# Performance work log

Measured on AMD Instinct MI355X. Metric: run time of the kernel, lower is better.

Reference implementation:

```python
import jax, jax.numpy as jnp
import numpy as np

SR = 44100
WT_LEN = 512
N_WT = 20
B, T = 16, 262144


def setup_inputs() -> dict:
    key = jax.random.key(0)
    k1, k2, k3, k4 = jax.random.split(key, 4)
    # realistic fundamental frequencies in [50, 500) Hz
    pitch = 50.0 + 450.0 * jax.random.uniform(k1, (B, T, 1), dtype=jnp.float32)
    amplitude = jax.random.uniform(k2, (B, T, 1), dtype=jnp.float32)
    attention = jax.random.uniform(k3, (B, T, N_WT), dtype=jnp.float32)
    # learned wavetables [N_WT, WT_LEN]; first 4 are fixed sine cycles, rest learnable noise
    i = np.arange(WT_LEN, dtype=np.float32)
    sines = np.stack([np.sin((c + 1) * 2 * np.pi * i / WT_LEN) for c in range(4)]).astype(np.float32)
    rest = 0.01 * np.asarray(jax.random.normal(k4, (N_WT - 4, WT_LEN)), dtype=np.float32)
    wt = np.concatenate([sines, rest], axis=0)
    # module enforces wt[-1] == wt[0] (periodic closure)
    wt[:, -1] = wt[:, 0]
    return {"pitch": pitch, "amplitude": amplitude, "attention": attention,
            "wavetables": jnp.asarray(wt)}


def reference(pitch, amplitude, attention, wavetables):
    L = wavetables.shape[1]
    # tanh applied to learnable tables only (indices >= 4)
    wt = jnp.concatenate([wavetables[:4], jnp.tanh(wavetables[4:])], axis=0)  # [K, L]
    freq = pitch[..., 0]                                   # [B, T]
    increment = freq / SR * L                              # [B, T]
    index = jnp.cumsum(increment, axis=-1) - increment[:, :1]
    index = index % L
    idx_low = jnp.floor(index)
    idx_high = jnp.ceil(index)
    alpha = index - idx_low                                # [B, T]
    il = idx_low.astype(jnp.int32)
    ih = (idx_high.astype(jnp.int32)) % L
    wt_t = wt.T                                            # [L, K]
    low = wt_t[il]                                         # [B, T, K] single gather for all tables
    high = wt_t[ih]                                        # [B, T, K]
    waveforms = low + alpha[..., None] * (high - low)      # [B, T, K]
    mixed = jnp.sum(waveforms * attention, axis=-1)        # [B, T]
    return (mixed[..., None] * amplitude)                  # [B, T, 1]
```

## Files before the change

kernel.cpp:

```cpp
#include <hip/hip_runtime.h>
#include <math.h>

#define WT_LEN 512
#define N_WT 20
#define B_ 16
#define T_ 262144
#define TOTAL (B_ * T_)
#define CHUNK 8192
#define NCHR 32
#define NCH  512
#define DTHREADS 1024

__device__ __forceinline__ float to_inc1(float x) {
    return (x / 44100.0f) * 512.0f;
}
__device__ __forceinline__ float4 to_inc4(float4 p) {
    float4 r;
    r.x = to_inc1(p.x); r.y = to_inc1(p.y);
    r.z = to_inc1(p.z); r.w = to_inc1(p.w);
    return r;
}

template <bool STORE_INC>
__global__ __launch_bounds__(DTHREADS) void up_kernel(
        const float* __restrict__ pitch, float* __restrict__ A13,
        float* __restrict__ incbuf) {
    __shared__ float red[2048];
    const int t = threadIdx.x;
    const size_t g0 = (size_t)blockIdx.x * CHUNK;

    const float4* p4 = (const float4*)(pitch + g0);
    float4 v0 = to_inc4(p4[2 * t]);
    float4 v1 = to_inc4(p4[2 * t + 1]);
    if (STORE_INC) {
        float4* q4 = (float4*)(incbuf + g0);
        q4[2 * t] = v0; q4[2 * t + 1] = v1;
    }
    float t0 = v0.x + v0.y, t1 = v0.z + v0.w;
    float t2 = v1.x + v1.y, t3 = v1.z + v1.w;
    red[t] = (t0 + t1) + (t2 + t3);
    __syncthreads();
    int off_prev = 0, off = 1024;
    for (int sz = 512; sz >= 1; sz >>= 1) {
        if (t < sz) red[off + t] = red[off_prev + 2 * t] + red[off_prev + 2 * t + 1];
        __syncthreads();
        off_prev = off; off += sz;
    }
    if (t == 0) A13[blockIdx.x] = red[2046];
}

__global__ void mid_kernel(const float* __restrict__ A13,
                           const float* __restrict__ pitch,
                           float* __restrict__ S13, float* __restrict__ X0) {
    int r = threadIdx.x;
    if (r >= B_) return;
    float l0[32], l1[16], l2[8], l3[4], l4[2], l5;
    for (int i = 0; i < 32; ++i) l0[i] = A13[r * 32 + i];
    for (int i = 0; i < 16; ++i) l1[i] = l0[2 * i] + l0[2 * i + 1];
    for (int i = 0; i < 8;  ++i) l2[i] = l1[2 * i] + l1[2 * i + 1];
    for (int i = 0; i < 4;  ++i) l3[i] = l2[2 * i] + l2[2 * i + 1];
    for (int i = 0; i < 2;  ++i) l4[i] = l3[2 * i] + l3[2 * i + 1];
    l5 = l4[0] + l4[1];

    float s4[2], s3[4], s2[8], s1[16], s0[32];
    s4[0] = l4[0]; s4[1] = l5;
    s3[0] = l3[0];
    for (int i = 0; i < 2; ++i) {
        s3[2 * i + 1] = s4[i];
        if (2 * i + 2 < 4) s3[2 * i + 2] = s4[i] + l3[2 * i + 2];
    }
    s2[0] = l2[0];
    for (int i = 0; i < 4; ++i) {
        s2[2 * i + 1] = s3[i];
        if (2 * i + 2 < 8) s2[2 * i + 2] = s3[i] + l2[2 * i + 2];
    }
    s1[0] = l1[0];
    for (int i = 0; i < 8; ++i) {
        s1[2 * i + 1] = s2[i];
        if (2 * i + 2 < 16) s1[2 * i + 2] = s2[i] + l1[2 * i + 2];
    }
    s0[0] = l0[0];
    for (int i = 0; i < 16; ++i) {
        s0[2 * i + 1] = s1[i];
        if (2 * i + 2 < 32) s0[2 * i + 2] = s1[i] + l0[2 * i + 2];
    }
    for (int i = 0; i < 32; ++i) S13[r * 32 + i] = s0[i];
    X0[r] = to_inc1(pitch[(size_t)r * T_]);
}

__constant__ int OFF[14] = {0, 8192, 12288, 14336, 15360, 15872, 16128,
                            16256, 16320, 16352, 16368, 16376, 16380, 16382};

template <bool FROM_INC>
__global__ __launch_bounds__(DTHREADS) void down_kernel(
        const float* __restrict__ src,
        const float* __restrict__ S13,
        float* __restrict__ sout) {
    __shared__ float a[16384];
    const int t = threadIdx.x;
    const size_t g0 = (size_t)blockIdx.x * CHUNK;

    const float4* p4 = (const float4*)(src + g0);
    float4 v0 = p4[2 * t], v1 = p4[2 * t + 1];
    if (!FROM_INC) { v0 = to_inc4(v0); v1 = to_inc4(v1); }
    ((float4*)a)[2 * t] = v0;
    ((float4*)a)[2 * t + 1] = v1;
    __syncthreads();

    for (int k = 1; k <= 12; ++k) {
        int m = CHUNK >> k;
        int bp = OFF[k - 1], b = OFF[k];
        for (int i = t; i < m; i += DTHREADS)
            a[b + i] = a[bp + 2 * i] + a[bp + 2 * i + 1];
        __syncthreads();
    }

    const float P = (blockIdx.x & (NCHR - 1)) ? S13[blockIdx.x - 1] : 0.0f;
    const float T13 = S13[blockIdx.x];

    if (t == 0) {
        a[OFF[12]]     = P + a[OFF[12]];
        a[OFF[12] + 1] = T13;
    }
    __syncthreads();
    for (int k = 11; k >= 0; --k) {
        int m = CHUNK >> k, half = m >> 1;
        int b = OFF[k], bn = OFF[k + 1];
        for (int i = t; i < half; i += DTHREADS) {
            float sn = a[bn + i];
            int j = 2 * i + 2;
            float av = (j < m) ? a[b + j] : 0.0f;
            a[b + 2 * i + 1] = sn;
            if (j < m) a[b + j] = sn + av;
        }
        if (t == 0) a[b] = P + a[b];
        __syncthreads();
    }

    float4* q4 = (float4*)(sout + g0);
    q4[2 * t]     = ((float4*)a)[2 * t];
    q4[2 * t + 1] = ((float4*)a)[2 * t + 1];
}

__global__ __launch_bounds__(256) void mix_kernel(
        float* io, const float* __restrict__ X0,
        const float* __restrict__ amp, const float* __restrict__ att,
        const float* __restrict__ wtg, int total) {
    __shared__ float wt_lds[WT_LEN * N_WT];
    for (int e = threadIdx.x; e < WT_LEN * N_WT; e += blockDim.x) {
        int c = e / WT_LEN;
        int i = e - c * WT_LEN;
        float v = wtg[e];
        if (c >= 4) v = tanhf(v);
        wt_lds[i * N_WT + c] = v;
    }
    __syncthreads();

    int gid = blockIdx.x * blockDim.x + threadIdx.x;
    if (gid >= total) return;

    int row = gid >> 18;
    float S  = io[gid];
    float y  = S - X0[row];

    float qf  = floorf(y * (1.0f / 512.0f));
    float idx = fmaf(-512.0f, qf, y);
    if (idx < 0.0f)    idx += 512.0f;
    if (idx >= 512.0f) idx -= 512.0f;

    float fl0   = floorf(idx);
    float alpha = idx - fl0;
    int il = ((int)fl0) & (WT_LEN - 1);
    int ih = (il + (alpha > 0.0f ? 1 : 0)) & (WT_LEN - 1);

    const float4* lo4 = (const float4*)(&wt_lds[il * N_WT]);
    const float4* hi4 = (const float4*)(&wt_lds[ih * N_WT]);
    const float4* a4  = (const float4*)(att + (size_t)gid * N_WT);

    float acc = 0.0f;
#pragma unroll
    for (int v = 0; v < 5; ++v) {
        float4 lo = lo4[v];
        float4 hi = hi4[v];
        float4 at = a4[v];
        acc += at.x * (lo.x + alpha * (hi.x - lo.x));
        acc += at.y * (lo.y + alpha * (hi.y - lo.y));
        acc += at.z * (lo.z + alpha * (hi.z - lo.z));
        acc += at.w * (lo.w + alpha * (hi.w - lo.w));
    }
    io[gid] = acc * amp[gid];
}

extern "C" void kernel_launch(void* const* d_in, const int* in_sizes, int n_in,
                              void* d_out, int out_size, void* d_ws, size_t ws_size,
                              hipStream_t stream) {
    const float* pitch = (const float*)d_in[0];
    const float* amp   = (const float*)d_in[1];
    const float* att   = (const float*)d_in[2];
    const float* wtg   = (const float*)d_in[3];
    float* S = (float*)d_out;

    float* A13 = (float*)d_ws;
    float* S13 = A13 + NCH;
    float* X0  = S13 + NCH;
    float* INC = A13 + 4096;
    const bool use_inc =
        ws_size >= (size_t)(4096 + TOTAL) * sizeof(float);

    if (use_inc) {
        up_kernel<true><<<NCH, DTHREADS, 0, stream>>>(pitch, A13, INC);
        mid_kernel<<<1, 64, 0, stream>>>(A13, pitch, S13, X0);
        down_kernel<true><<<NCH, DTHREADS, 0, stream>>>(INC, S13, S);
    } else {
        up_kernel<false><<<NCH, DTHREADS, 0, stream>>>(pitch, A13, nullptr);
        mid_kernel<<<1, 64, 0, stream>>>(A13, pitch, S13, X0);
        down_kernel<false><<<NCH, DTHREADS, 0, stream>>>(pitch, S13, S);
    }
    mix_kernel<<<(TOTAL + 255) / 256, 256, 0, stream>>>(S, X0, amp, att, wtg,
                                                        TOTAL);
}
```

Baseline: 565.0 us.

## Restructure scan to per-thread register sums and precompute wavetable once

The down-sweep scan now keeps each thread's 8 increments in registers and scans only the 1024 per-thread partial sums in a 2048-float LDS buffer, instead of a full 16K-float LDS tree over 8192 elements. The INC intermediate buffer is dropped, so pitch is reread and converted on the fly rather than written and reread. Wavetable tanh and transpose move into the single-block mid kernel, which writes them to workspace. The mix kernel becomes a persistent grid of 1024 blocks of 512 threads that bulk-copies the prepared table into LDS once per block. These changes aim to cut LDS traffic, barrier count, global memory traffic and per-block table setup, at the cost of extra work in the serial mid kernel.

```diff
diff --git a/kernel.cpp b/kernel.cpp
--- a/kernel.cpp
+++ b/kernel.cpp
@@ -9,7 +9,6 @@
 #define CHUNK 8192
 #define NCHR 32
 #define NCH  512
-#define DTHREADS 1024
 
 __device__ __forceinline__ float to_inc1(float x) {
     return (x / 44100.0f) * 512.0f;
@@ -21,10 +20,8 @@
     return r;
 }
 
-template <bool STORE_INC>
-__global__ __launch_bounds__(DTHREADS) void up_kernel(
-        const float* __restrict__ pitch, float* __restrict__ A13,
-        float* __restrict__ incbuf) {
+__global__ __launch_bounds__(1024) void up_kernel(
+        const float* __restrict__ pitch, float* __restrict__ A13) {
     __shared__ float red[2048];
     const int t = threadIdx.x;
     const size_t g0 = (size_t)blockIdx.x * CHUNK;
@@ -32,10 +29,6 @@
     const float4* p4 = (const float4*)(pitch + g0);
     float4 v0 = to_inc4(p4[2 * t]);
     float4 v1 = to_inc4(p4[2 * t + 1]);
-    if (STORE_INC) {
-        float4* q4 = (float4*)(incbuf + g0);
-        q4[2 * t] = v0; q4[2 * t + 1] = v1;
-    }
     float t0 = v0.x + v0.y, t1 = v0.z + v0.w;
     float t2 = v1.x + v1.y, t3 = v1.z + v1.w;
     red[t] = (t0 + t1) + (t2 + t3);
@@ -49,146 +42,161 @@
     if (t == 0) A13[blockIdx.x] = red[2046];
 }
 
-__global__ void mid_kernel(const float* __restrict__ A13,
-                           const float* __restrict__ pitch,
-                           float* __restrict__ S13, float* __restrict__ X0) {
+__global__ __launch_bounds__(1024) void mid_kernel(
+        const float* __restrict__ A13, const float* __restrict__ pitch,
+        const float* __restrict__ wtg, float* __restrict__ S13,
+        float* __restrict__ X0, float* __restrict__ WTT) {
     int r = threadIdx.x;
-    if (r >= B_) return;
-    float l0[32], l1[16], l2[8], l3[4], l4[2], l5;
-    for (int i = 0; i < 32; ++i) l0[i] = A13[r * 32 + i];
-    for (int i = 0; i < 16; ++i) l1[i] = l0[2 * i] + l0[2 * i + 1];
-    for (int i = 0; i < 8;  ++i) l2[i] = l1[2 * i] + l1[2 * i + 1];
-    for (int i = 0; i < 4;  ++i) l3[i] = l2[2 * i] + l2[2 * i + 1];
-    for (int i = 0; i < 2;  ++i) l4[i] = l3[2 * i] + l3[2 * i + 1];
-    l5 = l4[0] + l4[1];
-
-    float s4[2], s3[4], s2[8], s1[16], s0[32];
-    s4[0] = l4[0]; s4[1] = l5;
-    s3[0] = l3[0];
-    for (int i = 0; i < 2; ++i) {
-        s3[2 * i + 1] = s4[i];
-        if (2 * i + 2 < 4) s3[2 * i + 2] = s4[i] + l3[2 * i + 2];
-    }
-    s2[0] = l2[0];
-    for (int i = 0; i < 4; ++i) {
-        s2[2 * i + 1] = s3[i];
-        if (2 * i + 2 < 8) s2[2 * i + 2] = s3[i] + l2[2 * i + 2];
-    }
-    s1[0] = l1[0];
-    for (int i = 0; i < 8; ++i) {
-        s1[2 * i + 1] = s2[i];
-        if (2 * i + 2 < 16) s1[2 * i + 2] = s2[i] + l1[2 * i + 2];
-    }
-    s0[0] = l0[0];
-    for (int i = 0; i < 16; ++i) {
-        s0[2 * i + 1] = s1[i];
-        if (2 * i + 2 < 32) s0[2 * i + 2] = s1[i] + l0[2 * i + 2];
-    }
-    for (int i = 0; i < 32; ++i) S13[r * 32 + i] = s0[i];
-    X0[r] = to_inc1(pitch[(size_t)r * T_]);
-}
-
-__constant__ int OFF[14] = {0, 8192, 12288, 14336, 15360, 15872, 16128,
-                            16256, 16320, 16352, 16368, 16376, 16380, 16382};
-
-template <bool FROM_INC>
-__global__ __launch_bounds__(DTHREADS) void down_kernel(
-        const float* __restrict__ src,
-        const float* __restrict__ S13,
-        float* __restrict__ sout) {
-    __shared__ float a[16384];
-    const int t = threadIdx.x;
-    const size_t g0 = (size_t)blockIdx.x * CHUNK;
-
-    const float4* p4 = (const float4*)(src + g0);
-    float4 v0 = p4[2 * t], v1 = p4[2 * t + 1];
-    if (!FROM_INC) { v0 = to_inc4(v0); v1 = to_inc4(v1); }
-    ((float4*)a)[2 * t] = v0;
-    ((float4*)a)[2 * t + 1] = v1;
-    __syncthreads();
-
-    for (int k = 1; k <= 12; ++k) {
-        int m = CHUNK >> k;
-        int bp = OFF[k - 1], b = OFF[k];
-        for (int i = t; i < m; i += DTHREADS)
-            a[b + i] = a[bp + 2 * i] + a[bp + 2 * i + 1];
-        __syncthreads();
-    }
-
-    const float P = (blockIdx.x & (NCHR - 1)) ? S13[blockIdx.x - 1] : 0.0f;
-    const float T13 = S13[blockIdx.x];
-
-    if (t == 0) {
-        a[OFF[12]]     = P + a[OFF[12]];
-        a[OFF[12] + 1] = T13;
-    }
-    __syncthreads();
-    for (int k = 11; k >= 0; --k) {
-        int m = CHUNK >> k, half = m >> 1;
-        int b = OFF[k], bn = OFF[k + 1];
-        for (int i = t; i < half; i += DTHREADS) {
-            float sn = a[bn + i];
-            int j = 2 * i + 2;
-            float av = (j < m) ? a[b + j] : 0.0f;
-            a[b + 2 * i + 1] = sn;
-            if (j < m) a[b + j] = sn + av;
-        }
-        if (t == 0) a[b] = P + a[b];
-        __syncthreads();
-    }
-
-    float4* q4 = (float4*)(sout + g0);
-    q4[2 * t]     = ((float4*)a)[2 * t];
-    q4[2 * t + 1] = ((float4*)a)[2 * t + 1];
-}
-
-__global__ __launch_bounds__(256) void mix_kernel(
-        float* io, const float* __restrict__ X0,
-        const float* __restrict__ amp, const float* __restrict__ att,
-        const float* __restrict__ wtg, int total) {
-    __shared__ float wt_lds[WT_LEN * N_WT];
-    for (int e = threadIdx.x; e < WT_LEN * N_WT; e += blockDim.x) {
+    if (r < B_) {
+        float l0[32], l1[16], l2[8], l3[4], l4[2], l5;
+        for (int i = 0; i < 32; ++i) l0[i] = A13[r * 32 + i];
+        for (int i = 0; i < 16; ++i) l1[i] = l0[2 * i] + l0[2 * i + 1];
+        for (int i = 0; i < 8;  ++i) l2[i] = l1[2 * i] + l1[2 * i + 1];
+        for (int i = 0; i < 4;  ++i) l3[i] = l2[2 * i] + l2[2 * i + 1];
+        for (int i = 0; i < 2;  ++i) l4[i] = l3[2 * i] + l3[2 * i + 1];
+        l5 = l4[0] + l4[1];
+
+        float s4[2], s3[4], s2[8], s1[16], s0[32];
+        s4[0] = l4[0]; s4[1] = l5;
+        s3[0] = l3[0];
+        for (int i = 0; i < 2; ++i) {
+            s3[2 * i + 1] = s4[i];
+            if (2 * i + 2 < 4) s3[2 * i + 2] = s4[i] + l3[2 * i + 2];
+        }
+        s2[0] = l2[0];
+        for (int i = 0; i < 4; ++i) {
+            s2[2 * i + 1] = s3[i];
+            if (2 * i + 2 < 8) s2[2 * i + 2] = s3[i] + l2[2 * i + 2];
+        }
+        s1[0] = l1[0];
+        for (int i = 0; i < 8; ++i) {
+            s1[2 * i + 1] = s2[i];
+            if (2 * i + 2 < 16) s1[2 * i + 2] = s2[i] + l1[2 * i + 2];
+        }
+        s0[0] = l0[0];
+        for (int i = 0; i < 16; ++i) {
+            s0[2 * i + 1] = s1[i];
+            if (2 * i + 2 < 32) s0[2 * i + 2] = s1[i] + l0[2 * i + 2];
+        }
+        for (int i = 0; i < 32; ++i) S13[r * 32 + i] = s0[i];
+        X0[r] = to_inc1(pitch[(size_t)r * T_]);
+    }
+    for (int e = threadIdx.x; e < WT_LEN * N_WT; e += 1024) {
         int c = e / WT_LEN;
         int i = e - c * WT_LEN;
         float v = wtg[e];
         if (c >= 4) v = tanhf(v);
-        wt_lds[i * N_WT + c] = v;
-    }
-    __syncthreads();
-
-    int gid = blockIdx.x * blockDim.x + threadIdx.x;
-    if (gid >= total) return;
-
-    int row = gid >> 18;
-    float S  = io[gid];
-    float y  = S - X0[row];
-
-    float qf  = floorf(y * (1.0f / 512.0f));
-    float idx = fmaf(-512.0f, qf, y);
-    if (idx < 0.0f)    idx += 512.0f;
-    if (idx >= 512.0f) idx -= 512.0f;
-
-    float fl0   = floorf(idx);
-    float alpha = idx - fl0;
-    int il = ((int)fl0) & (WT_LEN - 1);
-    int ih = (il + (alpha > 0.0f ? 1 : 0)) & (WT_LEN - 1);
-
-    const float4* lo4 = (const float4*)(&wt_lds[il * N_WT]);
-    const float4* hi4 = (const float4*)(&wt_lds[ih * N_WT]);
-    const float4* a4  = (const float4*)(att + (size_t)gid * N_WT);
-
-    float acc = 0.0f;
+        WTT[i * N_WT + c] = v;
+    }
+}
+
+__global__ __launch_bounds__(1024) void down_kernel(
+        const float* __restrict__ pitch, const float* __restrict__ S13,
+        float* __restrict__ sout) {
+    __shared__ float a[2048];
+    const int t = threadIdx.x;
+    const int c = blockIdx.x;
+    const size_t g0 = (size_t)c * CHUNK;
+
+    const float4* p4 = (const float4*)(pitch + g0);
+    float4 va = to_inc4(p4[2 * t]);
+    float4 vb = to_inc4(p4[2 * t + 1]);
+    float x0 = va.x, x2 = va.z, x4 = vb.x, x6 = vb.z;
+    float t0 = va.x + va.y, t1 = va.z + va.w;
+    float t2 = vb.x + vb.y, t3 = vb.z + vb.w;
+    float u0 = t0 + t1, u1 = t2 + t3;
+    a[t] = u0 + u1;
+    __syncthreads();
+
+    int bp = 0, b = 1024;
+    for (int sz = 512; sz >= 2; sz >>= 1) {
+        if (t < sz) a[b + t] = a[bp + 2 * t] + a[bp + 2 * t + 1];
+        __syncthreads();
+        bp = b; b += sz;
+    }
+
+    const float P   = (c & (NCHR - 1)) ? S13[c - 1] : 0.0f;
+    const float T13 = S13[c];
+    if (t == 0) {
+        a[2044] = P + a[2044];
+        a[2045] = T13;
+    }
+    __syncthreads();
+
+    const int offk[10] = {0, 1024, 1536, 1792, 1920, 1984, 2016, 2032, 2040, 2044};
+    for (int k = 11; k >= 3; --k) {
+        int m = 1 << (13 - k), half = m >> 1;
+        int bk = offk[k - 3], bn = offk[k - 2];
+        if (t < half) {
+            float sn = a[bn + t];
+            int j = 2 * t + 2;
+            float av = (j < m) ? a[bk + j] : 0.0f;
+            a[bk + 2 * t + 1] = sn;
+            if (j < m) a[bk + j] = sn + av;
+        }
+        if (t == 0) a[bk] = P + a[bk];
+        __syncthreads();
+    }
+
+    float S3prev = t ? a[t - 1] : P;
+    float s3t = a[t];
+    float s1a = S3prev + t0;
+    float s2a = S3prev + u0;
+    float s1c = s2a + t2;
+    (void)t1; (void)t3; (void)u1;
+
+    float4* q4 = (float4*)(sout + g0);
+    q4[2 * t]     = make_float4(S3prev + x0, s1a, s1a + x2, s2a);
+    q4[2 * t + 1] = make_float4(s2a + x4, s1c, s1c + x6, s3t);
+}
+
+__global__ __launch_bounds__(512) void mix_kernel(
+        float* io, const float* __restrict__ X0,
+        const float* __restrict__ amp, const float* __restrict__ att,
+        const float* __restrict__ WTT, int ntiles) {
+    __shared__ float wt_lds[WT_LEN * N_WT];
+    {
+        const float4* src = (const float4*)WTT;
+        float4* dst = (float4*)wt_lds;
 #pragma unroll
-    for (int v = 0; v < 5; ++v) {
-        float4 lo = lo4[v];
-        float4 hi = hi4[v];
-        float4 at = a4[v];
-        acc += at.x * (lo.x + alpha * (hi.x - lo.x));
-        acc += at.y * (lo.y + alpha * (hi.y - lo.y));
-        acc += at.z * (lo.z + alpha * (hi.z - lo.z));
-        acc += at.w * (lo.w + alpha * (hi.w - lo.w));
-    }
-    io[gid] = acc * amp[gid];
+        for (int r = 0; r < 5; ++r)
+            dst[threadIdx.x + 512 * r] = src[threadIdx.x + 512 * r];
+    }
+    __syncthreads();
+
+    for (int tile = blockIdx.x; tile < ntiles; tile += gridDim.x) {
+        int gid = tile * 512 + threadIdx.x;
+        int row = gid >> 18;
+        float S = io[gid];
+        float y = S - X0[row];
+
+        float qf  = floorf(y * (1.0f / 512.0f));
+        float idx = fmaf(-512.0f, qf, y);
+        if (idx < 0.0f)    idx += 512.0f;
+        if (idx >= 512.0f) idx -= 512.0f;
+
+        float fl0   = floorf(idx);
+        float alpha = idx - fl0;
+        int il = ((int)fl0) & (WT_LEN - 1);
+        int ih = (il + (alpha > 0.0f ? 1 : 0)) & (WT_LEN - 1);
+
+        const float4* lo4 = (const float4*)(&wt_lds[il * N_WT]);
+        const float4* hi4 = (const float4*)(&wt_lds[ih * N_WT]);
+        const float4* a4  = (const float4*)(att + (size_t)gid * N_WT);
+
+        float acc = 0.0f;
+#pragma unroll
+        for (int v = 0; v < 5; ++v) {
+            float4 lo = lo4[v];
+            float4 hi = hi4[v];
+            float4 at = a4[v];
+            acc += at.x * (lo.x + alpha * (hi.x - lo.x));
+            acc += at.y * (lo.y + alpha * (hi.y - lo.y));
+            acc += at.z * (lo.z + alpha * (hi.z - lo.z));
+            acc += at.w * (lo.w + alpha * (hi.w - lo.w));
+        }
+        io[gid] = acc * amp[gid];
+    }
 }
 
 extern "C" void kernel_launch(void* const* d_in, const int* in_sizes, int n_in,
@@ -203,19 +211,11 @@
     float* A13 = (float*)d_ws;
     float* S13 = A13 + NCH;
     float* X0  = S13 + NCH;
-    float* INC = A13 + 4096;
-    const bool use_inc =
-        ws_size >= (size_t)(4096 + TOTAL) * sizeof(float);
-
-    if (use_inc) {
-        up_kernel<true><<<NCH, DTHREADS, 0, stream>>>(pitch, A13, INC);
-        mid_kernel<<<1, 64, 0, stream>>>(A13, pitch, S13, X0);
-        down_kernel<true><<<NCH, DTHREADS, 0, stream>>>(INC, S13, S);
-    } else {
-        up_kernel<false><<<NCH, DTHREADS, 0, stream>>>(pitch, A13, nullptr);
-        mid_kernel<<<1, 64, 0, stream>>>(A13, pitch, S13, X0);
-        down_kernel<false><<<NCH, DTHREADS, 0, stream>>>(pitch, S13, S);
-    }
-    mix_kernel<<<(TOTAL + 255) / 256, 256, 0, stream>>>(S, X0, amp, att, wtg,
-                                                        TOTAL);
-}
+    float* WTT = X0 + 64;
+
+    up_kernel<<<NCH, 1024, 0, stream>>>(pitch, A13);
+    mid_kernel<<<1, 1024, 0, stream>>>(A13, pitch, wtg, S13, X0, WTT);
+    down_kernel<<<NCH, 1024, 0, stream>>>(pitch, S13, S);
+    mix_kernel<<<1024, 512, 0, stream>>>(S, X0, amp, att, WTT,
+                                         TOTAL / 512);
+}
```

New measurement: 501.3 us. -11.3%, faster.
